# Kernel optimization log

Measured on AMD Instinct MI355X. Metric: run time of the kernel, lower is better.

The kernel has to match this reference:

```python
import jax, jax.numpy as jnp
import numpy as np

EPS = 1e-7  # keras.backend.epsilon()
B, U, F = 1024, 256, 31
D = 1 + U + F  # features dim after concat


def setup_inputs() -> dict:
    key = jax.random.key(0)
    ks = jax.random.split(key, 9)
    s = 1.0 / np.sqrt(D)
    return {
        "last_cell": jax.random.uniform(ks[0], (B, U), dtype=jnp.float32),
        "input_precipitation": jax.random.uniform(ks[1], (B,), dtype=jnp.float32),
        "input_other_features": jax.random.normal(ks[2], (B, F), dtype=jnp.float32),
        "W_i": jax.random.normal(ks[3], (D, U), dtype=jnp.float32) * s,
        "b_i": jnp.zeros((U,), dtype=jnp.float32),
        "W_r": jax.random.normal(ks[4], (D, U * U), dtype=jnp.float32) * s,
        "b_r": jnp.zeros((U * U,), dtype=jnp.float32),
        "W_o": jax.random.normal(ks[5], (D, U), dtype=jnp.float32) * s,
        "b_o": jnp.zeros((U,), dtype=jnp.float32),
    }


def reference(last_cell, input_precipitation, input_other_features,
              W_i, b_i, W_r, b_r, W_o, b_o):
    # L1-normalize last cell state (mass fractions)
    l1 = jnp.sum(jnp.abs(last_cell), axis=-1, keepdims=True) + EPS
    last_cell_hat = last_cell / l1
    p = input_precipitation[:, None]  # [B,1]
    features = jnp.concatenate([p, last_cell_hat, input_other_features], axis=-1)  # [B,D]

    # input gate: sigmoid then L1-normalized across units (mass-conserving split)
    ig = jax.nn.sigmoid(features @ W_i + b_i)
    ig = ig / jnp.sum(jnp.abs(ig), axis=-1, keepdims=True)

    # redistribution matrix: relu, reshape [B,U,U], L1-normalize each row
    R = jax.nn.relu(features @ W_r + b_r).reshape(-1, U, U)
    R = R / jnp.sum(jnp.abs(R), axis=-1, keepdims=True)

    # output gate: sigmoid
    og = jax.nn.sigmoid(features @ W_o + b_o)

    cell_in = ig * p                                   # [B,U]
    cell_sys = jnp.einsum('bu,buv->bv', last_cell, R)  # batched (1xU)@(UxU)
    candidate = cell_in + cell_sys
    output = og * candidate
    cell = (1.0 - og) * candidate
    return (cell, output)
```

## Files before the change

### kernel.cpp

```cpp
#include <hip/hip_runtime.h>


#define EPS_L1 1e-7f

constexpr int BB  = 1024;
constexpr int U   = 256;
constexpr int F   = 31;
constexpr int D   = 1 + U + F;
constexpr int NBV = BB * U;
constexpr int NCH = D / 32;
constexpr int UIMGB = NCH * 16384;
constexpr size_t WTB_BYTES  = (size_t)258 * UIMGB;
constexpr size_t FEAT_BYTES = (size_t)BB * D * 2;

typedef float f32x4 __attribute__((ext_vector_type(4)));
typedef short bf16x8 __attribute__((ext_vector_type(8)));

__device__ __forceinline__ unsigned f2bf(float x) {
  union { float f; unsigned u; } v; v.f = x;
  unsigned r = v.u + 0x7FFFu + ((v.u >> 16) & 1u);
  return r >> 16;
}

#define GLDS16(gp, lp)                                                        \
  __builtin_amdgcn_global_load_lds(                                          \
      (const __attribute__((address_space(1))) void*)(gp),                   \
      (__attribute__((address_space(3))) void*)(lp), 16, 0, 0)

#define MFMA16(a, b, c) __builtin_amdgcn_mfma_f32_16x16x32_bf16((a), (b), (c), 0, 0, 0)

__global__ __launch_bounds__(256) void k_prep(
    const float* __restrict__ lc, const float* __restrict__ p,
    const float* __restrict__ other,
    const float* __restrict__ Wi, const float* __restrict__ Wr,
    const float* __restrict__ Wo,
    short* __restrict__ WtB, short* __restrict__ featImg,
    float* __restrict__ cell_sys) {
  __shared__ unsigned tw[256][17];
  __shared__ float inv_s[64];
  const int bid = blockIdx.x, t = threadIdx.x;

  if (bid < 2322) {
    const int u = bid / 9, c = bid % 9;
    const float* src; long ld;
    if (u < 256)       { src = Wr + (size_t)u * 256; ld = 65536; }
    else if (u == 256) { src = Wi; ld = 256; }
    else               { src = Wo; ld = 256; }

    const int kp = t >> 4, f = t & 15;
    const float* r0 = src + (size_t)(c * 32 + 2 * kp) * ld;
    const float* r1 = r0 + ld;
#pragma unroll
    for (int i = 0; i < 4; ++i) {
      const int v0 = f * 4 + i * 64;
      const float4 a = *(const float4*)(r0 + v0);
      const float4 b = *(const float4*)(r1 + v0);
      tw[v0 + 0][kp] = f2bf(a.x) | (f2bf(b.x) << 16);
      tw[v0 + 1][kp] = f2bf(a.y) | (f2bf(b.y) << 16);
      tw[v0 + 2][kp] = f2bf(a.z) | (f2bf(b.z) << 16);
      tw[v0 + 3][kp] = f2bf(a.w) | (f2bf(b.w) << 16);
    }
    __syncthreads();

    const int lane = t & 63, wave = t >> 6;
    const int g = lane >> 4, l15 = lane & 15;
    short* dst = WtB + (size_t)u * 73728 + (size_t)c * 16 * 512;
#pragma unroll
    for (int ii = 0; ii < 4; ++ii) {
      const int n0 = wave * 4 + ii;
      const int row = n0 * 16 + l15;
      union { unsigned u4[4]; bf16x8 h; } cv;
#pragma unroll
      for (int j = 0; j < 4; ++j) cv.u4[j] = tw[row][g * 4 + j];
      *(bf16x8*)(dst + (size_t)n0 * 512 + lane * 8) = cv.h;
    }
  } else if (bid < 2338) {
    const int mb = bid - 2322;
    const int b0 = mb * 64;
    const int row = t >> 2, q = t & 3;
    const float4* lp = (const float4*)(lc + (size_t)(b0 + row) * 256 + q * 64);
    float s = 0.f;
#pragma unroll
    for (int j = 0; j < 16; ++j) {
      const float4 v = lp[j];
      s += fabsf(v.x) + fabsf(v.y) + fabsf(v.z) + fabsf(v.w);
    }
    s += __shfl_xor(s, 1, 64);
    s += __shfl_xor(s, 2, 64);
    if (q == 0) inv_s[row] = 1.f / (s + EPS_L1);
    __syncthreads();
#pragma unroll
    for (int i = 0; i < 9; ++i) {
      const int idx = i * 256 + t;
      const int reg = idx >> 6, l = idx & 63;
      const int c = reg >> 2, mt = reg & 3;
      const int lrow = mt * 16 + (l & 15);
      const int grow = b0 + lrow;
      const int k0 = c * 32 + (l >> 4) * 8;
      bf16x8 h;
#pragma unroll
      for (int j = 0; j < 8; ++j) {
        const int k = k0 + j;
        float v;
        if (k == 0) v = p[grow];
        else if (k <= 256) v = lc[(size_t)grow * 256 + (k - 1)] * inv_s[lrow];
        else v = other[(size_t)grow * 31 + (k - 257)];
        h[j] = (short)f2bf(v);
      }
      *(bf16x8*)(featImg + (size_t)mb * 18432 + (size_t)reg * 512 + l * 8) = h;
    }
  } else {
    float4* cs4 = (float4*)cell_sys;
    const int base = (bid - 2338) * 8192 + t;
    const float4 z = {0.f, 0.f, 0.f, 0.f};
#pragma unroll
    for (int k2 = 0; k2 < 32; ++k2) cs4[base + k2 * 256] = z;
  }
}

__global__ __launch_bounds__(512, 2) void k_heavyR8(
    const short* __restrict__ featImg, const short* __restrict__ WtB,
    const float* __restrict__ lc, const float* __restrict__ br,
    float* __restrict__ cell_sys) {
  __shared__ short aT[36864];
  __shared__ float rsum[2][128][4];
  __shared__ float lcs[8][128];

  const int t = threadIdx.x, lane = t & 63, wave = t >> 6;
  const int cq = wave & 3, rh = wave >> 2;
  const int quad = lane >> 4, l15 = lane & 15;
  const int bid = blockIdx.x;
  const int Mb = bid >> 5, ug = bid & 31;
  const int b0 = Mb * 128, u0 = ug * 8;

  {
    const char* gA = (const char*)featImg + (size_t)Mb * 73728;
    char* lA = (char*)aT;
#pragma unroll
    for (int i = 0; i < 9; ++i)
      GLDS16(gA + i * 8192 + t * 16, lA + i * 8192 + t * 16);
  }

  if (t < 128) {
    const float* lp = lc + (size_t)(b0 + t) * 256 + u0;
    const float4 v0 = *(const float4*)(lp);
    const float4 v1 = *(const float4*)(lp + 4);
    lcs[0][t] = v0.x; lcs[1][t] = v0.y; lcs[2][t] = v0.z; lcs[3][t] = v0.w;
    lcs[4][t] = v1.x; lcs[5][t] = v1.y; lcs[6][t] = v1.z; lcs[7][t] = v1.w;
  }

  const char* aB = (const char*)aT + rh * 36864 + lane * 16;
  const char* bB = (const char*)WtB + (size_t)u0 * UIMGB + cq * 4096 + lane * 16;

  f32x4 acc[4][4], outa[4][4];
#pragma unroll
  for (int m = 0; m < 4; ++m)
#pragma unroll
    for (int n = 0; n < 4; ++n)
#pragma unroll
      for (int r = 0; r < 4; ++r) { acc[m][n][r] = 0.f; outa[m][n][r] = 0.f; }

  bf16x8 bfr[3][4];
#pragma unroll
  for (int n = 0; n < 4; ++n) bfr[0][n] = *(const bf16x8*)(bB + n * 1024);
#pragma unroll
  for (int n = 0; n < 4; ++n) bfr[1][n] = *(const bf16x8*)(bB + 16384 + n * 1024);

  __syncthreads();

  bf16x8 afr[2][4];
#pragma unroll
  for (int m = 0; m < 4; ++m) afr[0][m] = *(const bf16x8*)(aB + m * 1024);

  for (int uu = 0; uu < 8; ++uu) {
    const int u = u0 + uu;
    float bv[4];

#pragma unroll
    for (int c = 0; c < 9; ++c) {
      if (c == 0) {
#pragma unroll
        for (int n = 0; n < 4; ++n)
          bv[n] = br[(size_t)u * 256 + cq * 64 + n * 16 + l15];
      }
#pragma unroll
      for (int n = 0; n < 4; ++n)
        bfr[(c + 2) % 3][n] = *(const bf16x8*)(bB + (c + 2) * 16384 + n * 1024);
      if (c < 8) {
#pragma unroll
        for (int m = 0; m < 4; ++m)
          afr[(c + 1) & 1][m] = *(const bf16x8*)(aB + (c + 1) * 4096 + m * 1024);
      }
#pragma unroll
      for (int m = 0; m < 4; ++m)
#pragma unroll
        for (int n = 0; n < 4; ++n)
          acc[m][n] = MFMA16(afr[c & 1][m], bfr[c % 3][n], acc[m][n]);
    }
    bB += UIMGB;

#pragma unroll
    for (int m = 0; m < 4; ++m) afr[0][m] = *(const bf16x8*)(aB + m * 1024);

    const int ub = uu & 1;
    float sm[4][4];
#pragma unroll
    for (int m = 0; m < 4; ++m)
#pragma unroll
      for (int r = 0; r < 4; ++r) {
        float sv = 0.f;
#pragma unroll
        for (int n = 0; n < 4; ++n) {
          const float rv = fmaxf(acc[m][n][r] + bv[n], 0.f);
          acc[m][n][r] = rv;
          sv += rv;
        }
        sm[m][r] = sv;
      }
#pragma unroll
    for (int msk = 1; msk < 16; msk <<= 1)
#pragma unroll
      for (int m = 0; m < 4; ++m)
#pragma unroll
        for (int r = 0; r < 4; ++r)
          sm[m][r] += __shfl_xor(sm[m][r], msk, 64);
    if (l15 == 0) {
#pragma unroll
      for (int m = 0; m < 4; ++m)
#pragma unroll
        for (int r = 0; r < 4; ++r)
          rsum[ub][rh * 64 + m * 16 + quad * 4 + r][cq] = sm[m][r];
    }
    __syncthreads();
#pragma unroll
    for (int m = 0; m < 4; ++m)
#pragma unroll
      for (int r = 0; r < 4; ++r) {
        const int row = rh * 64 + m * 16 + quad * 4 + r;
        const float4 rv = *(const float4*)&rsum[ub][row][0];
        const float tot = (rv.x + rv.y) + (rv.z + rv.w);
        const float alpha = lcs[uu][row] * __builtin_amdgcn_rcpf(tot);
#pragma unroll
        for (int n = 0; n < 4; ++n) {
          outa[m][n][r] = fmaf(alpha, acc[m][n][r], outa[m][n][r]);
          acc[m][n][r] = 0.f;
        }
      }
  }

#pragma unroll
  for (int m = 0; m < 4; ++m)
#pragma unroll
    for (int r = 0; r < 4; ++r) {
      const int grow = b0 + rh * 64 + m * 16 + quad * 4 + r;
#pragma unroll
      for (int n = 0; n < 4; ++n)
        atomicAdd(&cell_sys[(size_t)grow * 256 + cq * 64 + n * 16 + l15],
                  outa[m][n][r]);
    }
}

__global__ __launch_bounds__(512, 2) void k_postR8(
    const short* __restrict__ featImg, const short* __restrict__ WtB,
    const float* __restrict__ bi, const float* __restrict__ bo,
    const float* __restrict__ p, const float* __restrict__ cell_sys,
    float* __restrict__ dout) {
  __shared__ short aT9[9 * 512];
  __shared__ float cs[16 * 256];
  __shared__ float rsum[16][12];
  __shared__ float ps[16];

  const int t = threadIdx.x, lane = t & 63, cg = t >> 6;
  const int quad = lane >> 4, l15 = lane & 15;
  const int mb16 = blockIdx.x, b0 = mb16 * 16;
  const int mb = mb16 >> 2, mt = mb16 & 3;

  {
    const char* gsrc = (const char*)featImg + (size_t)mb * 36864 + mt * 1024;
    char* ldst = (char*)aT9;
    GLDS16(gsrc + (size_t)(t >> 6) * 4096 + (t & 63) * 16, ldst + t * 16);
    if (t < 64)
      GLDS16(gsrc + (size_t)8 * 4096 + t * 16, ldst + 8192 + t * 16);
  }
  if (t < 16) ps[t] = p[b0 + t];

  {
    const f32x4* pp = (const f32x4*)(cell_sys + (size_t)b0 * 256);
    ((f32x4*)cs)[t] = pp[t];
    ((f32x4*)cs)[512 + t] = pp[512 + t];
  }

  f32x4 acc[2];
#pragma unroll
  for (int n = 0; n < 2; ++n)
#pragma unroll
    for (int r = 0; r < 4; ++r) acc[n][r] = 0.f;

  const char* bptr = (const char*)WtB + (size_t)256 * UIMGB + cg * 2048 + lane * 16;
  bf16x8 cb0 = *(const bf16x8*)(bptr);
  bf16x8 cb1 = *(const bf16x8*)(bptr + 1024);
  bf16x8 nb0 = *(const bf16x8*)(bptr + 16384);
  bf16x8 nb1 = *(const bf16x8*)(bptr + 16384 + 1024);
  bptr += 32768;

  __syncthreads();

  float ig0[4], ig1[4], og0[4], og1[4];

#pragma unroll
  for (int g = 0; g < 2; ++g) {
    const float* bias = (g == 0) ? bi : bo;
    const float bv0 = bias[cg * 32 + l15];
    const float bv1 = bias[cg * 32 + 16 + l15];
#pragma unroll
    for (int c = 0; c < 9; ++c) {
      const bf16x8 pb0 = *(const bf16x8*)(bptr);
      const bf16x8 pb1 = *(const bf16x8*)(bptr + 1024);
      bptr += 16384;
      const bf16x8 a0 = *(const bf16x8*)((const char*)aT9 + c * 1024 + lane * 16);
      acc[0] = MFMA16(a0, cb0, acc[0]);
      acc[1] = MFMA16(a0, cb1, acc[1]);
      cb0 = nb0; cb1 = nb1; nb0 = pb0; nb1 = pb1;
    }

#pragma unroll
    for (int r = 0; r < 4; ++r) {
      const float v0 = 1.f / (1.f + __expf(-(acc[0][r] + bv0)));
      const float v1 = 1.f / (1.f + __expf(-(acc[1][r] + bv1)));
      if (g == 0) { ig0[r] = v0; ig1[r] = v1; }
      else        { og0[r] = v0; og1[r] = v1; }
      acc[0][r] = 0.f;
      acc[1][r] = 0.f;
    }

    if (g == 0) {
      float sm[4];
#pragma unroll
      for (int r = 0; r < 4; ++r) sm[r] = ig0[r] + ig1[r];
#pragma unroll
      for (int msk = 1; msk < 16; msk <<= 1)
#pragma unroll
        for (int r = 0; r < 4; ++r)
          sm[r] += __shfl_xor(sm[r], msk, 64);
      if (l15 == 0) {
#pragma unroll
        for (int r = 0; r < 4; ++r)
          rsum[quad * 4 + r][cg] = sm[r];
      }
      __syncthreads();
#pragma unroll
      for (int r = 0; r < 4; ++r) {
        const int row = quad * 4 + r;
        const float4 ra = *(const float4*)&rsum[row][0];
        const float4 rb = *(const float4*)&rsum[row][4];
        const float inv = 1.f / (((ra.x + ra.y) + (ra.z + ra.w)) +
                                 ((rb.x + rb.y) + (rb.z + rb.w)));
        ig0[r] *= inv;
        ig1[r] *= inv;
      }
    }
  }

#pragma unroll
  for (int r = 0; r < 4; ++r) {
    const int row = quad * 4 + r;
    const float pr = ps[row];
    const int ci = row * 256 + cg * 32 + l15;
    const size_t base = (size_t)(b0 + row) * 256 + cg * 32 + l15;
    {
      const float cand = fmaf(ig0[r], pr, cs[ci]);
      dout[base] = (1.f - og0[r]) * cand;
      dout[NBV + base] = og0[r] * cand;
    }
    {
      const float cand = fmaf(ig1[r], pr, cs[ci + 16]);
      dout[base + 16] = (1.f - og1[r]) * cand;
      dout[NBV + base + 16] = og1[r] * cand;
    }
  }
}

extern "C" void kernel_launch(void* const* d_in, const int* in_sizes, int n_in,
                              void* d_out, int out_size, void* d_ws, size_t ws_size,
                              hipStream_t stream) {
  const float* lc    = (const float*)d_in[0];
  const float* p     = (const float*)d_in[1];
  const float* other = (const float*)d_in[2];
  const float* Wi    = (const float*)d_in[3];
  const float* bi    = (const float*)d_in[4];
  const float* Wr    = (const float*)d_in[5];
  const float* br    = (const float*)d_in[6];
  const float* Wo    = (const float*)d_in[7];
  const float* bo    = (const float*)d_in[8];
  float* out = (float*)d_out;

  char* wsb = (char*)d_ws;
  short* WtB      = (short*)wsb;
  short* featImg  = (short*)(wsb + WTB_BYTES);
  float* cell_sys = (float*)(wsb + WTB_BYTES + FEAT_BYTES);

  k_prep<<<2346, 256, 0, stream>>>(lc, p, other, Wi, Wr, Wo, WtB, featImg, cell_sys);
  k_heavyR8<<<256, 512, 0, stream>>>(featImg, WtB, lc, br, cell_sys);
  k_postR8<<<64, 512, 0, stream>>>(featImg, WtB, bi, bo, p, cell_sys, out);
}
```

Measured before the change: 216.8 us.

## Stage R-weight tiles through LDS with triple-buffered global_load_lds

Before, each wave loaded the W_r B-fragments straight from global memory into registers, so the two row-half waves fetched the same data twice. Now the block streams each B chunk once into a three-slot LDS ring using global_load_lds, and syncs each chunk with a vmcnt-wait plus barrier. The A and B fragments are then read from LDS right before the MFMAs, replacing the register double and triple buffering. This cuts redundant global traffic and register pressure, but adds a block-wide barrier per K-chunk and exposes LDS read latency. The roughly 130 KB of LDS per block also leaves room for only one block per CU.

```diff
diff --git a/kernel.cpp b/kernel.cpp
--- a/kernel.cpp
+++ b/kernel.cpp
@@ -12,6 +12,7 @@
 constexpr int UIMGB = NCH * 16384;
 constexpr size_t WTB_BYTES  = (size_t)258 * UIMGB;
 constexpr size_t FEAT_BYTES = (size_t)BB * D * 2;
+constexpr int HEAVY_DYN_LDS = 73728 + 3 * 16384;
 
 typedef float f32x4 __attribute__((ext_vector_type(4)));
 typedef short bf16x8 __attribute__((ext_vector_type(8)));
@@ -20,6 +21,20 @@
   union { float f; unsigned u; } v; v.f = x;
   unsigned r = v.u + 0x7FFFu + ((v.u >> 16) & 1u);
   return r >> 16;
+}
+
+__device__ __forceinline__ void barrier_lgkm() {
+  asm volatile("s_waitcnt lgkmcnt(0)" ::: "memory");
+  __builtin_amdgcn_sched_barrier(0);
+  __builtin_amdgcn_s_barrier();
+  __builtin_amdgcn_sched_barrier(0);
+}
+
+__device__ __forceinline__ void wait_vm2_barrier() {
+  asm volatile("s_waitcnt vmcnt(2)" ::: "memory");
+  __builtin_amdgcn_sched_barrier(0);
+  __builtin_amdgcn_s_barrier();
+  __builtin_amdgcn_sched_barrier(0);
 }
 
 #define GLDS16(gp, lp)                                                        \
@@ -118,13 +133,16 @@
   }
 }
 
-__global__ __launch_bounds__(512, 2) void k_heavyR8(
+__global__ __launch_bounds__(512, 2) void k_heavyR11(
     const short* __restrict__ featImg, const short* __restrict__ WtB,
     const float* __restrict__ lc, const float* __restrict__ br,
     float* __restrict__ cell_sys) {
-  __shared__ short aT[36864];
+  extern __shared__ char dyn[];
   __shared__ float rsum[2][128][4];
   __shared__ float lcs[8][128];
+
+  char* aT = dyn;
+  char* bS = dyn + 73728;
 
   const int t = threadIdx.x, lane = t & 63, wave = t >> 6;
   const int cq = wave & 3, rh = wave >> 2;
@@ -135,12 +153,10 @@
 
   {
     const char* gA = (const char*)featImg + (size_t)Mb * 73728;
-    char* lA = (char*)aT;
 #pragma unroll
     for (int i = 0; i < 9; ++i)
-      GLDS16(gA + i * 8192 + t * 16, lA + i * 8192 + t * 16);
-  }
-
+      GLDS16(gA + i * 8192 + t * 16, aT + i * 8192 + t * 16);
+  }
   if (t < 128) {
     const float* lp = lc + (size_t)(b0 + t) * 256 + u0;
     const float4 v0 = *(const float4*)(lp);
@@ -148,9 +164,14 @@
     lcs[0][t] = v0.x; lcs[1][t] = v0.y; lcs[2][t] = v0.z; lcs[3][t] = v0.w;
     lcs[4][t] = v1.x; lcs[5][t] = v1.y; lcs[6][t] = v1.z; lcs[7][t] = v1.w;
   }
-
-  const char* aB = (const char*)aT + rh * 36864 + lane * 16;
-  const char* bB = (const char*)WtB + (size_t)u0 * UIMGB + cq * 4096 + lane * 16;
+  const char* bG = (const char*)WtB + (size_t)u0 * UIMGB;
+#pragma unroll
+  for (int s0 = 0; s0 < 2; ++s0) {
+    GLDS16(bG + s0 * 16384 + t * 16, bS + s0 * 16384 + t * 16);
+    GLDS16(bG + s0 * 16384 + 8192 + t * 16, bS + s0 * 16384 + 8192 + t * 16);
+  }
+
+  const char* aB = aT + rh * 36864 + lane * 16;
 
   f32x4 acc[4][4], outa[4][4];
 #pragma unroll
@@ -160,47 +181,55 @@
 #pragma unroll
       for (int r = 0; r < 4; ++r) { acc[m][n][r] = 0.f; outa[m][n][r] = 0.f; }
 
-  bf16x8 bfr[3][4];
-#pragma unroll
-  for (int n = 0; n < 4; ++n) bfr[0][n] = *(const bf16x8*)(bB + n * 1024);
-#pragma unroll
-  for (int n = 0; n < 4; ++n) bfr[1][n] = *(const bf16x8*)(bB + 16384 + n * 1024);
-
-  __syncthreads();
-
-  bf16x8 afr[2][4];
-#pragma unroll
-  for (int m = 0; m < 4; ++m) afr[0][m] = *(const bf16x8*)(aB + m * 1024);
-
+  int cc = 0;
   for (int uu = 0; uu < 8; ++uu) {
     const int u = u0 + uu;
     float bv[4];
 
 #pragma unroll
-    for (int c = 0; c < 9; ++c) {
+    for (int c = 0; c < 9; ++c, ++cc) {
+      wait_vm2_barrier();
+
       if (c == 0) {
 #pragma unroll
         for (int n = 0; n < 4; ++n)
           bv[n] = br[(size_t)u * 256 + cq * 64 + n * 16 + l15];
       }
-#pragma unroll
-      for (int n = 0; n < 4; ++n)
-        bfr[(c + 2) % 3][n] = *(const bf16x8*)(bB + (c + 2) * 16384 + n * 1024);
-      if (c < 8) {
-#pragma unroll
-        for (int m = 0; m < 4; ++m)
-          afr[(c + 1) & 1][m] = *(const bf16x8*)(aB + (c + 1) * 4096 + m * 1024);
-      }
-#pragma unroll
-      for (int m = 0; m < 4; ++m)
-#pragma unroll
-        for (int n = 0; n < 4; ++n)
-          acc[m][n] = MFMA16(afr[c & 1][m], bfr[c % 3][n], acc[m][n]);
-    }
-    bB += UIMGB;
-
-#pragma unroll
-    for (int m = 0; m < 4; ++m) afr[0][m] = *(const bf16x8*)(aB + m * 1024);
+      {
+        const size_t off = (size_t)(cc + 2) * 16384;
+        char* dst = bS + ((cc + 2) % 3) * 16384;
+        GLDS16(bG + off + t * 16, dst + t * 16);
+        GLDS16(bG + off + 8192 + t * 16, dst + 8192 + t * 16);
+      }
+
+      const char* bP = bS + (cc % 3) * 16384 + cq * 4096 + lane * 16;
+      const char* aP = aB + c * 4096;
+      const bf16x8 a0 = *(const bf16x8*)(aP);
+      const bf16x8 a1 = *(const bf16x8*)(aP + 1024);
+      const bf16x8 a2 = *(const bf16x8*)(aP + 2048);
+      const bf16x8 a3 = *(const bf16x8*)(aP + 3072);
+      const bf16x8 b0 = *(const bf16x8*)(bP);
+      const bf16x8 b1 = *(const bf16x8*)(bP + 1024);
+      const bf16x8 b2 = *(const bf16x8*)(bP + 2048);
+      const bf16x8 b3 = *(const bf16x8*)(bP + 3072);
+
+      acc[0][0] = MFMA16(a0, b0, acc[0][0]);
+      acc[0][1] = MFMA16(a0, b1, acc[0][1]);
+      acc[0][2] = MFMA16(a0, b2, acc[0][2]);
+      acc[0][3] = MFMA16(a0, b3, acc[0][3]);
+      acc[1][0] = MFMA16(a1, b0, acc[1][0]);
+      acc[1][1] = MFMA16(a1, b1, acc[1][1]);
+      acc[1][2] = MFMA16(a1, b2, acc[1][2]);
+      acc[1][3] = MFMA16(a1, b3, acc[1][3]);
+      acc[2][0] = MFMA16(a2, b0, acc[2][0]);
+      acc[2][1] = MFMA16(a2, b1, acc[2][1]);
+      acc[2][2] = MFMA16(a2, b2, acc[2][2]);
+      acc[2][3] = MFMA16(a2, b3, acc[2][3]);
+      acc[3][0] = MFMA16(a3, b0, acc[3][0]);
+      acc[3][1] = MFMA16(a3, b1, acc[3][1]);
+      acc[3][2] = MFMA16(a3, b2, acc[3][2]);
+      acc[3][3] = MFMA16(a3, b3, acc[3][3]);
+    }
 
     const int ub = uu & 1;
     float sm[4][4];
@@ -231,7 +260,7 @@
         for (int r = 0; r < 4; ++r)
           rsum[ub][rh * 64 + m * 16 + quad * 4 + r][cq] = sm[m][r];
     }
-    __syncthreads();
+    barrier_lgkm();
 #pragma unroll
     for (int m = 0; m < 4; ++m)
 #pragma unroll
@@ -399,7 +428,15 @@
   short* featImg  = (short*)(wsb + WTB_BYTES);
   float* cell_sys = (float*)(wsb + WTB_BYTES + FEAT_BYTES);
 
+  static bool attr_done = false;
+  if (!attr_done) {
+    hipFuncSetAttribute(reinterpret_cast<const void*>(k_heavyR11),
+                        hipFuncAttributeMaxDynamicSharedMemorySize,
+                        HEAVY_DYN_LDS);
+    attr_done = true;
+  }
+
   k_prep<<<2346, 256, 0, stream>>>(lc, p, other, Wi, Wr, Wo, WtB, featImg, cell_sys);
-  k_heavyR8<<<256, 512, 0, stream>>>(featImg, WtB, lc, br, cell_sys);
+  k_heavyR11<<<256, 512, HEAVY_DYN_LDS, stream>>>(featImg, WtB, lc, br, cell_sys);
   k_postR8<<<64, 512, 0, stream>>>(featImg, WtB, bi, bo, p, cell_sys, out);
 }
```

New measurement: 216.2 us. No clear change (-0.3%).
